# Optimization experiments

Measured on AMD Instinct MI355X. Metric: run time of the kernel, lower is better.

## Reference

```python
import jax, jax.numpy as jnp
import numpy as np

GEOM_W = 0.01
N_ITERS = 5
HUBER_DELTA = 1.345
LM_EPS = 1e-6


def _skew(w):
    x, y, z = w[..., 0], w[..., 1], w[..., 2]
    o = jnp.zeros_like(x)
    return jnp.stack([
        jnp.stack([o, -z, y], -1),
        jnp.stack([z, o, -x], -1),
        jnp.stack([-y, x, o], -1)], -2)


def _se3_exp(xi):
    # xi: [B,6] = (v, w), translation first (matches Jt = [I | -skew(X)])
    v, w = xi[..., :3], xi[..., 3:]
    t2 = jnp.sum(w * w, -1)[..., None, None]
    small = t2 < 1e-8
    t2s = jnp.where(small, 1.0, t2)
    th = jnp.sqrt(t2s)
    A = jnp.where(small, 1.0 - t2 / 6.0, jnp.sin(th) / th)
    Bc = jnp.where(small, 0.5 - t2 / 24.0, (1.0 - jnp.cos(th)) / t2s)
    Cc = jnp.where(small, 1.0 / 6.0 - t2 / 120.0, (th - jnp.sin(th)) / (t2s * th))
    wx = _skew(w)
    wx2 = jnp.matmul(wx, wx)
    I3 = jnp.eye(3, dtype=xi.dtype)
    R = I3 + A * wx + Bc * wx2
    V = I3 + Bc * wx + Cc * wx2
    t = jnp.einsum('bij,bj->bi', V, v)
    top = jnp.concatenate([R, t[..., None]], -1)           # [B,3,4]
    bot = jnp.broadcast_to(jnp.array([0.0, 0.0, 0.0, 1.0], dtype=xi.dtype), top[..., :1, :].shape)
    return jnp.concatenate([top, bot], -2)                 # [B,4,4]


def _grid_sample(img, gx, gy):
    # bilinear, padding_mode='zeros', align_corners=True; img [B,C,H,W], gx/gy [B,H,W] in [-1,1]
    B, C, H, W = img.shape
    x = (gx + 1.0) * 0.5 * (W - 1)
    y = (gy + 1.0) * 0.5 * (H - 1)
    x0 = jnp.floor(x)
    y0 = jnp.floor(y)
    fx1 = x - x0
    fy1 = y - y0
    flat = img.reshape(B, C, H * W)

    def corner(xi, yi, wgt):
        inb = (xi >= 0) & (xi <= W - 1) & (yi >= 0) & (yi <= H - 1)
        xc = jnp.clip(xi, 0, W - 1).astype(jnp.int32)
        yc = jnp.clip(yi, 0, H - 1).astype(jnp.int32)
        idx = (yc * W + xc).reshape(B, 1, H * W)
        vals = jnp.take_along_axis(flat, idx, axis=2).reshape(B, C, H, W)
        return vals * (wgt * inb)[:, None]

    return (corner(x0, y0, (1 - fx1) * (1 - fy1)) + corner(x0 + 1, y0, fx1 * (1 - fy1))
            + corner(x0, y0 + 1, (1 - fx1) * fy1) + corner(x0 + 1, y0 + 1, fx1 * fy1))


def _feature_gradient(img):
    # central differences with replicate padding: [B,C,H,W] -> (d/dx, d/dy)
    px = jnp.pad(img, ((0, 0), (0, 0), (0, 0), (1, 1)), mode='edge')
    py = jnp.pad(img, ((0, 0), (0, 0), (1, 1), (0, 0)), mode='edge')
    dx = 0.5 * (px[..., 2:] - px[..., :-2])
    dy = 0.5 * (py[..., 2:, :] - py[..., :-2, :])
    return dx, dy


def _forward(pose, I0, I1, invD0, invD1, intrinsics, depth0, depth1):
    B, C, H, W = I0.shape
    dt = I0.dtype
    fxv = intrinsics[:, 0][:, None, None]
    fyv = intrinsics[:, 1][:, None, None]
    cx = intrinsics[:, 2][:, None, None]
    cy = intrinsics[:, 3][:, None, None]
    vv, uu = jnp.meshgrid(jnp.arange(H, dtype=dt), jnp.arange(W, dtype=dt), indexing='ij')
    d1 = depth1[:, 0]
    # back-projected points in frame 1: [B,H,W,3]
    X1 = jnp.stack([d1 * (uu - cx) / fxv, d1 * (vv - cy) / fyv, d1], -1)
    dI0x, dI0y = _feature_gradient(I0)
    dD0x, dD0y = _feature_gradient(depth0)
    eye3 = jnp.eye(3, dtype=dt)
    lam = GEOM_W
    for _ in range(N_ITERS):
        R = pose[:, :3, :3]
        t = pose[:, :3, 3]
        X0 = jnp.einsum('bij,bhwj->bhwi', R, X1) + t[:, None, None, :]   # [B,H,W,3]
        x, y, z = X0[..., 0], X0[..., 1], X0[..., 2]
        vproj = z > 1e-6
        zs = jnp.where(vproj, z, 1.0)
        u0 = fxv * x / zs + cx
        v0 = fyv * y / zs + cy
        d = z
        inb = (u0 > 0) & (u0 < W - 1) & (v0 > 0) & (v0 < H - 1)
        valid = inb & vproj & (depth0[:, 0] > 0) & (depth1[:, 0] > 0)    # [B,H,W]
        zero = jnp.zeros_like(zs)
        row0 = jnp.stack([fxv / zs + zero, zero, -fxv * x / (zs * zs)], -1)
        row1 = jnp.stack([zero, fyv / zs + zero, -fyv * y / (zs * zs)], -1)
        Jp = jnp.stack([row0, row1], -2)                                  # [B,H,W,2,3]
        Jt = jnp.concatenate([jnp.broadcast_to(eye3, (B, H, W, 3, 3)), -_skew(X0)], -1)  # [B,H,W,3,6]
        Jw = jnp.einsum('bhwij,bhwjk->bhwik', Jp, Jt)                     # [B,H,W,2,6]
        gx = jnp.clip((u0 / (W - 1) - 0.5) * 2.0, -2.0, 2.0)
        gy = jnp.clip((v0 / (H - 1) - 0.5) * 2.0, -2.0, 2.0)
        I0w = _grid_sample(I0, gx, gy)
        r_I = I1 - I0w                                                    # [B,C,H,W]
        D0w = _grid_sample(depth0, gx, gy)
        r_Z = d[:, None] - D0w                                            # [B,1,H,W]
        gI = jnp.stack([_grid_sample(dI0x, gx, gy), _grid_sample(dI0y, gx, gy)], -1)  # [B,C,H,W,2]
        J_I = jnp.einsum('bchwn,bhwnk->bchwk', gI, Jw)                    # [B,C,H,W,6]
        gD = jnp.stack([_grid_sample(dD0x, gx, gy), _grid_sample(dD0y, gx, gy)], -1)  # [B,1,H,W,2]
        J_Z = jnp.einsum('bchwn,bhwnk->bchwk', gD, Jw) - Jt[..., 2, :][:, None]       # [B,1,H,W,6]
        vexp = jnp.broadcast_to(valid[:, None], (B, C + 1, H, W)).reshape(B, -1).astype(dt)
        J = jnp.concatenate([J_I.reshape(B, -1, 6), lam * J_Z.reshape(B, -1, 6)], 1) * vexp[..., None]
        r = jnp.concatenate([r_I.reshape(B, -1), lam * r_Z.reshape(B, -1)], 1) * vexp
        ar = jnp.abs(r)
        wts = jnp.where(ar <= HUBER_DELTA, 1.0, HUBER_DELTA / jnp.maximum(ar, 1e-8))  # Huber M-estimator
        JtJ = jnp.einsum('bnk,bnl->bkl', J, wts[..., None] * J)           # [B,6,6]
        Hs = JtJ + LM_EPS * jnp.eye(6, dtype=dt)                          # LM damping
        Rhs = jnp.einsum('bnk,bn->bk', J, wts * r)                        # [B,6]
        xi = jnp.linalg.solve(Hs, Rhs[..., None])[..., 0]                 # batched 6x6 solve
        pose = jnp.matmul(_se3_exp(xi), pose)                             # left-multiplicative retraction
    return pose


def setup_inputs() -> dict:
    key = jax.random.key(0)
    ks = jax.random.split(key, 5)
    B, C, H, W = 4, 16, 240, 320
    I0 = jax.random.normal(ks[0], (B, C, H, W), jnp.float32)
    I1 = jax.random.normal(ks[1], (B, C, H, W), jnp.float32)
    depth0 = jax.random.uniform(ks[2], (B, 1, H, W), jnp.float32, 0.5, 2.0)
    depth1 = jax.random.uniform(ks[3], (B, 1, H, W), jnp.float32, 0.5, 2.0)
    invD0 = 1.0 / depth0
    invD1 = 1.0 / depth1
    intrinsics = jnp.tile(jnp.array([[250.0, 250.0, (W - 1) / 2.0, (H - 1) / 2.0]], jnp.float32), (B, 1))
    xi0 = 0.01 * jax.random.normal(ks[4], (B, 6), jnp.float32)
    pose = _se3_exp(xi0)
    return {'pose': pose, 'I0': I0, 'I1': I1, 'invD0': invD0, 'invD1': invD1,
            'intrinsics': intrinsics, 'depth0': depth0, 'depth1': depth1}


def reference(pose, I0, I1, invD0, invD1, intrinsics, depth0, depth1):
    return _forward(pose, I0, I1, invD0, invD1, intrinsics, depth0, depth1)
```

## Files before the change

### kernel.cpp

```cpp
#include <hip/hip_runtime.h>
#include <math.h>

#define B_   4
#define C_   16
#define H_   240
#define W_   320
#define HW_  (H_*W_)
#define TPB  256
#define NBLK (HW_/TPB)
#define NACC 27
#define GEOM_W_ 0.01f
#define HUBER_  1.345f
#define LM_EPS_ 1e-6
#define N_ITERS_ 5

typedef float f4u __attribute__((ext_vector_type(4), aligned(4)));
typedef float f2u __attribute__((ext_vector_type(2), aligned(4)));

__global__ void dia_init(const float* __restrict__ pose_in, float* __restrict__ pose,
                         double* __restrict__ acc, int* __restrict__ tick) {
    const int i = threadIdx.x;
    if (i < N_ITERS_ * B_ * NACC) acc[i] = 0.0;
    if (i < N_ITERS_ * B_) tick[i] = 0;
    if (i < B_ * 16) pose[i] = pose_in[i];
}

__device__ __forceinline__ void samp12v(const float* __restrict__ base,
                                        int x0, bool interior, int xm1, int xp2,
                                        int ro0, int rum, int rdp,
                                        float w00, float w10, float w01, float w11,
                                        float& sv, float& sdx, float& sdy)
{
    const float* r0 = base + ro0;
    const float* r1 = r0 + W_;
    float A0, A1, A2, A3, B0, B1, B2, B3;
    if (interior) {
        f4u a = *(const f4u*)(r0 + x0 - 1);
        f4u c = *(const f4u*)(r1 + x0 - 1);
        A0 = a[0]; A1 = a[1]; A2 = a[2]; A3 = a[3];
        B0 = c[0]; B1 = c[1]; B2 = c[2]; B3 = c[3];
    } else {
        A0 = r0[xm1]; A1 = r0[x0]; A2 = r0[x0+1]; A3 = r0[xp2];
        B0 = r1[xm1]; B1 = r1[x0]; B2 = r1[x0+1]; B3 = r1[xp2];
    }
    f2u uv = *(const f2u*)(base + rum + x0);
    f2u dv = *(const f2u*)(base + rdp + x0);
    sv  = w00*A1 + w10*A2 + w01*B1 + w11*B2;
    sdx = 0.5f*( w00*(A2-A0) + w10*(A3-A1) + w01*(B2-B0) + w11*(B3-B1) );
    sdy = 0.5f*( w00*(B1-uv[0]) + w10*(B2-uv[1]) + w01*(dv[0]-A1) + w11*(dv[1]-A2) );
}

__device__ __attribute__((noinline)) void solve_update(const double* __restrict__ S,
                                                       float* __restrict__ P)
{
    double Hm[6][7];
    {
        int k = 0;
        double JtJ[6][6];
        for (int i = 0; i < 6; ++i)
            for (int j = i; j < 6; ++j) { JtJ[i][j] = S[k]; JtJ[j][i] = S[k]; ++k; }
        for (int i = 0; i < 6; ++i) {
            for (int j = 0; j < 6; ++j) Hm[i][j] = JtJ[i][j] + (i == j ? LM_EPS_ : 0.0);
            Hm[i][6] = S[21 + i];
        }
    }
    double xi[6];
    for (int col = 0; col < 6; ++col) {
        int piv = col; double mx = fabs(Hm[col][col]);
        for (int r2 = col+1; r2 < 6; ++r2) { double a = fabs(Hm[r2][col]); if (a > mx) { mx = a; piv = r2; } }
        if (piv != col)
            for (int j2 = col; j2 < 7; ++j2) { double tmp = Hm[col][j2]; Hm[col][j2] = Hm[piv][j2]; Hm[piv][j2] = tmp; }
        const double inv = 1.0 / Hm[col][col];
        for (int r2 = col+1; r2 < 6; ++r2) {
            const double f = Hm[r2][col] * inv;
            for (int j2 = col; j2 < 7; ++j2) Hm[r2][j2] -= f * Hm[col][j2];
        }
    }
    for (int r2 = 5; r2 >= 0; --r2) {
        double s = Hm[r2][6];
        for (int j2 = r2+1; j2 < 6; ++j2) s -= Hm[r2][j2] * xi[j2];
        xi[r2] = s / Hm[r2][r2];
    }

    const double vx = xi[0], vy = xi[1], vz = xi[2];
    const double wx = xi[3], wy = xi[4], wz = xi[5];
    const double t2 = wx*wx + wy*wy + wz*wz;
    double A, Bc, Cc;
    if (t2 < 1e-8) {
        A  = 1.0 - t2 / 6.0;
        Bc = 0.5 - t2 / 24.0;
        Cc = 1.0/6.0 - t2 / 120.0;
    } else {
        const double th = sqrt(t2);
        const double sth = sin(th), cth = cos(th);
        A  = sth / th;
        Bc = (1.0 - cth) / t2;
        Cc = (th - sth) / (t2 * th);
    }
    const double Wm[9] = { 0.0, -wz,  wy,
                           wz,  0.0, -wx,
                          -wy,  wx,  0.0 };
    double W2[9];
    for (int i = 0; i < 3; ++i)
        for (int j = 0; j < 3; ++j) {
            double s = 0.0;
            for (int k = 0; k < 3; ++k) s += Wm[i*3+k] * Wm[k*3+j];
            W2[i*3+j] = s;
        }
    double Rm[9], Vm[9];
    for (int i = 0; i < 9; ++i) {
        const double id = (i % 4 == 0) ? 1.0 : 0.0;
        Rm[i] = id + A  * Wm[i] + Bc * W2[i];
        Vm[i] = id + Bc * Wm[i] + Cc * W2[i];
    }
    const double tx = Vm[0]*vx + Vm[1]*vy + Vm[2]*vz;
    const double ty = Vm[3]*vx + Vm[4]*vy + Vm[5]*vz;
    const double tz = Vm[6]*vx + Vm[7]*vy + Vm[8]*vz;

    double Pm[16];
    for (int i = 0; i < 16; ++i) Pm[i] = (double)P[i];
    double E[16] = { Rm[0], Rm[1], Rm[2], tx,
                     Rm[3], Rm[4], Rm[5], ty,
                     Rm[6], Rm[7], Rm[8], tz,
                     0.0,   0.0,   0.0,   1.0 };
    double out[16];
    for (int i = 0; i < 4; ++i)
        for (int j = 0; j < 4; ++j) {
            double s = 0.0;
            for (int k = 0; k < 4; ++k) s += E[i*4+k] * Pm[k*4+j];
            out[i*4+j] = s;
        }
    for (int i = 0; i < 16; ++i) P[i] = (float)out[i];
}

__global__ __launch_bounds__(256, 5) void dia_reduce(
    float* __restrict__ pose,
    const float* __restrict__ I0,
    const float* __restrict__ I1,
    const float* __restrict__ intr,
    const float* __restrict__ depth0,
    const float* __restrict__ depth1,
    double* __restrict__ acc,
    int* __restrict__ tick)
{
    const int b = blockIdx.y;
    const int p = blockIdx.x * TPB + threadIdx.x;

    const float fxv = intr[b*4+0], fyv = intr[b*4+1];
    const float cx  = intr[b*4+2], cy  = intr[b*4+3];
    const float ifx = 1.0f / fxv,  ify = 1.0f / fyv;

    float Rm[9], tv[3];
#pragma unroll
    for (int i = 0; i < 3; ++i) {
#pragma unroll
        for (int j = 0; j < 3; ++j) Rm[i*3+j] = pose[b*16 + i*4 + j];
        tv[i] = pose[b*16 + i*4 + 3];
    }

    const float* d0p = depth0 + b * HW_;
    const float* d1p = depth1 + b * HW_;
    const float* I0b = I0 + (size_t)b * C_ * HW_;
    const float* I1b = I1 + (size_t)b * C_ * HW_;

    float Jw0[6] = {0,0,0,0,0,0};
    float Jw1[6] = {0,0,0,0,0,0};
    float JZ[6]  = {0,0,0,0,0,0};
    float Ga = 0.f, Gb = 0.f, Gd = 0.f, grx = 0.f, gry = 0.f, wz2 = 0.f, rZ = 0.f;

    {
        const int v = p / W_;
        const int u = p - v * W_;

        const float d1 = d1p[p];
        const float d0 = d0p[p];
        const float X1x = d1 * ((float)u - cx) * ifx;
        const float X1y = d1 * ((float)v - cy) * ify;
        const float x = Rm[0]*X1x + Rm[1]*X1y + Rm[2]*d1 + tv[0];
        const float y = Rm[3]*X1x + Rm[4]*X1y + Rm[5]*d1 + tv[1];
        const float z = Rm[6]*X1x + Rm[7]*X1y + Rm[8]*d1 + tv[2];

        const bool vproj = z > 1e-6f;
        const float zs = vproj ? z : 1.0f;
        const float iz = 1.0f / zs;
        const float u0 = fxv * x * iz + cx;
        const float v0 = fyv * y * iz + cy;
        const bool inb = (u0 > 0.f) && (u0 < (float)(W_-1)) && (v0 > 0.f) && (v0 < (float)(H_-1));
        const bool valid = inb && vproj && (d0 > 0.f) && (d1 > 0.f);

        if (valid) {
            const float x0f = floorf(u0), y0f = floorf(v0);
            const int x0 = (int)x0f, y0 = (int)y0f;
            const float fx1 = u0 - x0f, fy1 = v0 - y0f;
            const float w00 = (1.f-fx1)*(1.f-fy1), w10 = fx1*(1.f-fy1);
            const float w01 = (1.f-fx1)*fy1,       w11 = fx1*fy1;
            const int xm1 = max(x0-1, 0), xp2 = min(x0+2, W_-1);
            const int ym1 = max(y0-1, 0), yp2 = min(y0+2, H_-1);
            const bool interior = (x0 >= 1) && (x0 <= W_-3);
            const int ro0 = y0 * W_;
            const int rum = ym1 * W_;
            const int rdp = yp2 * W_;

            {
                const float a0 = fxv * iz;
                const float a2 = -fxv * x * iz * iz;
                const float b1 = fyv * iz;
                const float b2 = -fyv * y * iz * iz;
                Jw0[0] = a0;           Jw0[1] = 0.f;   Jw0[2] = a2;
                Jw0[3] = a2 * y;       Jw0[4] = a0*z - a2*x; Jw0[5] = -a0*y;
                Jw1[0] = 0.f;          Jw1[1] = b1;    Jw1[2] = b2;
                Jw1[3] = -b1*z + b2*y; Jw1[4] = -b2*x; Jw1[5] = b1*x;
            }

            {
                float D0w, dDx, dDy;
                samp12v(d0p, x0, interior, xm1, xp2, ro0, rum, rdp,
                        w00, w10, w01, w11, D0w, dDx, dDy);
                rZ = z - D0w;
#pragma unroll
                for (int j = 0; j < 6; ++j) JZ[j] = dDx*Jw0[j] + dDy*Jw1[j];
                JZ[2] -= 1.f; JZ[3] -= y; JZ[4] += x;
                const float arz = fabsf(GEOM_W_ * rZ);
                const float wzw = (arz <= HUBER_) ? 1.f : HUBER_ / fmaxf(arz, 1e-8f);
                wz2 = wzw * GEOM_W_ * GEOM_W_;
            }

#pragma unroll 2
            for (int c = 0; c < C_; ++c) {
                float Iw, gxc, gyc;
                samp12v(I0b + (size_t)c * HW_, x0, interior, xm1, xp2, ro0, rum, rdp,
                        w00, w10, w01, w11, Iw, gxc, gyc);
                const float r = I1b[(size_t)c * HW_ + p] - Iw;
                const float ar = fabsf(r);
                const float wc = (ar <= HUBER_) ? 1.f : HUBER_ / fmaxf(ar, 1e-8f);
                Ga  += wc * gxc * gxc;
                Gb  += wc * gxc * gyc;
                Gd  += wc * gyc * gyc;
                grx += wc * r * gxc;
                gry += wc * r * gyc;
            }
        }
    }

    __shared__ float sred[4][NACC];
    const int lane = threadIdx.x & 63;
    const int wid  = threadIdx.x >> 6;
    int k = 0;
#pragma unroll
    for (int i = 0; i < 6; ++i) {
#pragma unroll
        for (int j = i; j < 6; ++j) {
            float vt = Ga * Jw0[i] * Jw0[j]
                     + Gb * (Jw0[i] * Jw1[j] + Jw1[i] * Jw0[j])
                     + Gd * Jw1[i] * Jw1[j]
                     + wz2 * JZ[i] * JZ[j];
#pragma unroll
            for (int off = 32; off > 0; off >>= 1) vt += __shfl_down(vt, off, 64);
            if (lane == 0) sred[wid][k] = vt;
            ++k;
        }
    }
#pragma unroll
    for (int i = 0; i < 6; ++i) {
        float vt = grx * Jw0[i] + gry * Jw1[i] + wz2 * rZ * JZ[i];
#pragma unroll
        for (int off = 32; off > 0; off >>= 1) vt += __shfl_down(vt, off, 64);
        if (lane == 0) sred[wid][21 + i] = vt;
    }
    __syncthreads();
    if (threadIdx.x < NACC) {
        const double s = (double)sred[0][threadIdx.x] + (double)sred[1][threadIdx.x]
                       + (double)sred[2][threadIdx.x] + (double)sred[3][threadIdx.x];
        atomicAdd(&acc[b * NACC + threadIdx.x], s);
    }
    __syncthreads();

    if (threadIdx.x == 0) {
        __threadfence();
        const int old = atomicAdd(&tick[b], 1);
        if (old == NBLK - 1) {
            __threadfence();
            double S[NACC];
            for (int i = 0; i < NACC; ++i)
                S[i] = atomicAdd(&acc[b * NACC + i], 0.0);
            solve_update(S, pose + b * 16);
        }
    }
}

extern "C" void kernel_launch(void* const* d_in, const int* in_sizes, int n_in,
                              void* d_out, int out_size, void* d_ws, size_t ws_size,
                              hipStream_t stream) {
    const float* pose_in = (const float*)d_in[0];
    const float* I0      = (const float*)d_in[1];
    const float* I1      = (const float*)d_in[2];
    const float* intr    = (const float*)d_in[5];
    const float* depth0  = (const float*)d_in[6];
    const float* depth1  = (const float*)d_in[7];

    float*  pose = (float*)d_out;
    double* acc  = (double*)d_ws;
    int*    tick = (int*)(acc + N_ITERS_ * B_ * NACC);

    hipLaunchKernelGGL(dia_init, dim3(1), dim3(576), 0, stream, pose_in, pose, acc, tick);
    for (int it = 0; it < N_ITERS_; ++it) {
        hipLaunchKernelGGL(dia_reduce, dim3(NBLK, B_), dim3(TPB), 0, stream,
                           pose, I0, I1, intr, depth0, depth1,
                           acc + (size_t)it * B_ * NACC, tick + (size_t)it * B_);
    }
}
```

Before: 433.6 us.

## Swizzle blocks across XCDs and batch four channel loads in interior path

Flattens the grid to one dimension and remaps block IDs so consecutive blocks on each XCD handle contiguous strips of the same batch image, aiming for better L2 locality across the chiplets. Splits the channel loop into an interior path that issues vector loads for four channels at once before computing, which increases memory-level parallelism, and a scalar fallback path for borders. Lowers the launch_bounds occupancy hint from 5 to 4 to give the batched loads more registers. The cost is higher register pressure and potentially lower occupancy.

```diff
diff --git a/kernel.cpp b/kernel.cpp
--- a/kernel.cpp
+++ b/kernel.cpp
@@ -13,6 +13,7 @@
 #define HUBER_  1.345f
 #define LM_EPS_ 1e-6
 #define N_ITERS_ 5
+#define NXCD 8
 
 typedef float f4u __attribute__((ext_vector_type(4), aligned(4)));
 typedef float f2u __attribute__((ext_vector_type(2), aligned(4)));
@@ -25,24 +26,16 @@
     if (i < B_ * 16) pose[i] = pose_in[i];
 }
 
-__device__ __forceinline__ void samp12v(const float* __restrict__ base,
-                                        int x0, bool interior, int xm1, int xp2,
+__device__ __forceinline__ void samp12s(const float* __restrict__ base,
+                                        int x0, int xm1, int xp2,
                                         int ro0, int rum, int rdp,
                                         float w00, float w10, float w01, float w11,
                                         float& sv, float& sdx, float& sdy)
 {
     const float* r0 = base + ro0;
     const float* r1 = r0 + W_;
-    float A0, A1, A2, A3, B0, B1, B2, B3;
-    if (interior) {
-        f4u a = *(const f4u*)(r0 + x0 - 1);
-        f4u c = *(const f4u*)(r1 + x0 - 1);
-        A0 = a[0]; A1 = a[1]; A2 = a[2]; A3 = a[3];
-        B0 = c[0]; B1 = c[1]; B2 = c[2]; B3 = c[3];
-    } else {
-        A0 = r0[xm1]; A1 = r0[x0]; A2 = r0[x0+1]; A3 = r0[xp2];
-        B0 = r1[xm1]; B1 = r1[x0]; B2 = r1[x0+1]; B3 = r1[xp2];
-    }
+    float A0 = r0[xm1], A1 = r0[x0], A2 = r0[x0+1], A3 = r0[xp2];
+    float B0 = r1[xm1], B1 = r1[x0], B2 = r1[x0+1], B3 = r1[xp2];
     f2u uv = *(const f2u*)(base + rum + x0);
     f2u dv = *(const f2u*)(base + rdp + x0);
     sv  = w00*A1 + w10*A2 + w01*B1 + w11*B2;
@@ -133,7 +126,7 @@
     for (int i = 0; i < 16; ++i) P[i] = (float)out[i];
 }
 
-__global__ __launch_bounds__(256, 5) void dia_reduce(
+__global__ __launch_bounds__(256, 4) void dia_reduce(
     float* __restrict__ pose,
     const float* __restrict__ I0,
     const float* __restrict__ I1,
@@ -143,8 +136,11 @@
     double* __restrict__ acc,
     int* __restrict__ tick)
 {
-    const int b = blockIdx.y;
-    const int p = blockIdx.x * TPB + threadIdx.x;
+    const int bid = blockIdx.x;
+    const int swz = (bid & (NXCD-1)) * (NBLK * B_ / NXCD) + (bid >> 3);
+    const int b     = swz / NBLK;
+    const int strip = swz - b * NBLK;
+    const int p = strip * TPB + threadIdx.x;
 
     const float fxv = intr[b*4+0], fyv = intr[b*4+1];
     const float cx  = intr[b*4+2], cy  = intr[b*4+3];
@@ -214,7 +210,7 @@
 
             {
                 float D0w, dDx, dDy;
-                samp12v(d0p, x0, interior, xm1, xp2, ro0, rum, rdp,
+                samp12s(d0p, x0, xm1, xp2, ro0, rum, rdp,
                         w00, w10, w01, w11, D0w, dDx, dDy);
                 rZ = z - D0w;
 #pragma unroll
@@ -225,19 +221,54 @@
                 wz2 = wzw * GEOM_W_ * GEOM_W_;
             }
 
-#pragma unroll 2
-            for (int c = 0; c < C_; ++c) {
-                float Iw, gxc, gyc;
-                samp12v(I0b + (size_t)c * HW_, x0, interior, xm1, xp2, ro0, rum, rdp,
-                        w00, w10, w01, w11, Iw, gxc, gyc);
-                const float r = I1b[(size_t)c * HW_ + p] - Iw;
-                const float ar = fabsf(r);
-                const float wc = (ar <= HUBER_) ? 1.f : HUBER_ / fmaxf(ar, 1e-8f);
-                Ga  += wc * gxc * gxc;
-                Gb  += wc * gxc * gyc;
-                Gd  += wc * gyc * gyc;
-                grx += wc * r * gxc;
-                gry += wc * r * gyc;
+            if (interior) {
+                const float* bp0 = I0b + ro0 + x0 - 1;
+                const float* bp1 = bp0 + W_;
+                const float* bpu = I0b + rum + x0;
+                const float* bpd = I0b + rdp + x0;
+                const float* i1p = I1b + p;
+                for (int cc = 0; cc < C_; cc += 4) {
+                    f4u a[4], c[4]; f2u uu[4], dd[4]; float i1v[4];
+#pragma unroll
+                    for (int q = 0; q < 4; ++q) {
+                        const size_t off = (size_t)(cc + q) * HW_;
+                        a[q]  = *(const f4u*)(bp0 + off);
+                        c[q]  = *(const f4u*)(bp1 + off);
+                        uu[q] = *(const f2u*)(bpu + off);
+                        dd[q] = *(const f2u*)(bpd + off);
+                        i1v[q] = i1p[off];
+                    }
+#pragma unroll
+                    for (int q = 0; q < 4; ++q) {
+                        const float Iw  = w00*a[q][1] + w10*a[q][2] + w01*c[q][1] + w11*c[q][2];
+                        const float gxc = 0.5f*( w00*(a[q][2]-a[q][0]) + w10*(a[q][3]-a[q][1])
+                                               + w01*(c[q][2]-c[q][0]) + w11*(c[q][3]-c[q][1]) );
+                        const float gyc = 0.5f*( w00*(c[q][1]-uu[q][0]) + w10*(c[q][2]-uu[q][1])
+                                               + w01*(dd[q][0]-a[q][1]) + w11*(dd[q][1]-a[q][2]) );
+                        const float r  = i1v[q] - Iw;
+                        const float ar = fabsf(r);
+                        const float wc = (ar <= HUBER_) ? 1.f : HUBER_ / fmaxf(ar, 1e-8f);
+                        Ga  += wc * gxc * gxc;
+                        Gb  += wc * gxc * gyc;
+                        Gd  += wc * gyc * gyc;
+                        grx += wc * r * gxc;
+                        gry += wc * r * gyc;
+                    }
+                }
+            } else {
+                for (int c = 0; c < C_; ++c) {
+                    float Iw, gxc, gyc;
+                    samp12s(I0b + (size_t)c * HW_, x0, xm1, xp2, ro0, rum, rdp,
+                            w00, w10, w01, w11, Iw, gxc, gyc);
+                    const float r = I1b[(size_t)c * HW_ + p] - Iw;
+                    const float ar = fabsf(r);
+                    const float wc = (ar <= HUBER_) ? 1.f : HUBER_ / fmaxf(ar, 1e-8f);
+                    Ga  += wc * gxc * gxc;
+                    Gb  += wc * gxc * gyc;
+                    Gd  += wc * gyc * gyc;
+                    grx += wc * r * gxc;
+                    gry += wc * r * gyc;
+                }
             }
         }
     }
@@ -304,7 +335,7 @@
 
     hipLaunchKernelGGL(dia_init, dim3(1), dim3(576), 0, stream, pose_in, pose, acc, tick);
     for (int it = 0; it < N_ITERS_; ++it) {
-        hipLaunchKernelGGL(dia_reduce, dim3(NBLK, B_), dim3(TPB), 0, stream,
+        hipLaunchKernelGGL(dia_reduce, dim3(NBLK * B_), dim3(TPB), 0, stream,
                            pose, I0, I1, intr, depth0, depth1,
                            acc + (size_t)it * B_ * NACC, tick + (size_t)it * B_);
     }
```

New measurement: 1.035 ms. +138.8%, slower.
